# Kernel tuning notes

Hardware: AMD Instinct MI355X
Metric: run time of the kernel (lower is better)

The kernel has to match this reference:

```python
import jax, jax.numpy as jnp
import numpy as np

N_NODES = 100000
N_EDGES = 1600000
IN_DIM, HID_DIM, OUT_DIM = 128, 128, 47
BN_EPS = 1e-5


def setup_inputs() -> dict:
    key = jax.random.key(0)
    ks = jax.random.split(key, 12)
    x = jax.random.normal(ks[0], (N_NODES, IN_DIM), dtype=jnp.float32)
    edge_index = jax.random.randint(ks[1], (2, N_EDGES), 0, N_NODES, dtype=jnp.int32)
    def glorot(k, fan_in, fan_out):
        s = jnp.sqrt(6.0 / (fan_in + fan_out))
        return jax.random.uniform(k, (fan_in, fan_out), jnp.float32, -s, s)
    return {
        "x": x,
        "edge_index": edge_index,
        "W0": glorot(ks[2], IN_DIM, HID_DIM), "b0": jnp.zeros((HID_DIM,), jnp.float32),
        "W1": glorot(ks[3], HID_DIM, HID_DIM), "b1": jnp.zeros((HID_DIM,), jnp.float32),
        "W2": glorot(ks[4], HID_DIM, OUT_DIM), "b2": jnp.zeros((OUT_DIM,), jnp.float32),
        "g0": jnp.ones((HID_DIM,), jnp.float32), "be0": jnp.zeros((HID_DIM,), jnp.float32),
        "g1": jnp.ones((HID_DIM,), jnp.float32), "be1": jnp.zeros((HID_DIM,), jnp.float32),
    }


def _gcn_norm(edge_index, n_nodes):
    # add self-loops, compute sym-normalized edge weights (PyG GCNConv default)
    loop = jnp.arange(n_nodes, dtype=edge_index.dtype)
    src = jnp.concatenate([edge_index[0], loop])
    dst = jnp.concatenate([edge_index[1], loop])
    deg = jax.ops.segment_sum(jnp.ones_like(dst, dtype=jnp.float32), dst,
                              num_segments=n_nodes)
    dinv = jnp.where(deg > 0, jax.lax.rsqrt(deg), 0.0)
    norm = dinv[src] * dinv[dst]  # [E + N]
    return src, dst, norm


def _conv(x, W, b, src, dst, norm, n_nodes):
    h = x @ W                                   # [N, d_out]
    msg = h[src] * norm[:, None]                # gather + scale
    out = jax.ops.segment_sum(msg, dst, num_segments=n_nodes)
    return out + b


def _batchnorm(h, gamma, beta):
    mean = jnp.mean(h, axis=0)
    var = jnp.mean(jnp.square(h - mean), axis=0)  # biased var (torch BN)
    return (h - mean) * jax.lax.rsqrt(var + BN_EPS) * gamma + beta


def reference(x, edge_index, W0, b0, W1, b1, W2, b2, g0, be0, g1, be1):
    n = x.shape[0]
    src, dst, norm = _gcn_norm(edge_index, n)
    h = _conv(x, W0, b0, src, dst, norm, n)
    h = jax.nn.relu(_batchnorm(h, g0, be0))     # dropout = identity (eval)
    h = _conv(h, W1, b1, src, dst, norm, n)
    h = jax.nn.relu(_batchnorm(h, g1, be1))
    h = _conv(h, W2, b2, src, dst, norm, n)
    return jax.nn.log_softmax(h, axis=-1)
```

## Files before the change

### kernel.cpp

```cpp
#include <hip/hip_runtime.h>
#include <math.h>

#define N_NODES 100000
#define N_EDGES 1600000
#define HID 128
#define OUTD 47
#define OSTR 64

#define NPB 128
#define NB 782
#define BCAP 2560
#define CHUNK 2048
#define NCHB 782
#define CWB 64

typedef short bf16x8 __attribute__((ext_vector_type(8)));
typedef float f32x4 __attribute__((ext_vector_type(4)));

__device__ inline unsigned short f2bf(float x) {
    union { float f; unsigned int u; } v; v.f = x;
    unsigned int r = v.u + 0x7fffu + ((v.u >> 16) & 1u);
    return (unsigned short)(r >> 16);
}
__device__ inline float bf_lo(unsigned int u) { return __uint_as_float(u << 16); }
__device__ inline float bf_hi(unsigned int u) { return __uint_as_float(u & 0xffff0000u); }

__device__ inline unsigned int cvt_pk_bf16(float lo, float hi) {
    unsigned int r;
    asm("v_cvt_pk_bf16_f32 %0, %1, %2" : "=v"(r) : "v"(lo), "v"(hi));
    return r;
}

__device__ inline unsigned int src_chunk(unsigned int s) {
    return (s * 42950u) >> 28;
}


__global__ __launch_bounds__(256) void binA_k(
    const int* __restrict__ src, const int* __restrict__ dst,
    int* __restrict__ gcur, unsigned int* __restrict__ binned,
    const float* __restrict__ W0, const float* __restrict__ W1, const float* __restrict__ W2,
    unsigned short* __restrict__ Wt0, unsigned short* __restrict__ Wt1,
    unsigned short* __restrict__ Wt2)
{
    __shared__ unsigned int sortedL[CHUNK];
    __shared__ unsigned short bucketOf[CHUNK];
    __shared__ int cntL[NB];
    __shared__ int excL[NB];
    __shared__ int curL[NB];
    __shared__ int gposL[NB];
    __shared__ int partial[256];

    int t = threadIdx.x;

    if (blockIdx.x >= NCHB) {
        int i = (blockIdx.x - NCHB) * 256 + t;
        if (i < 16384) {
            int n = i >> 7, k = i & 127;
            Wt0[i] = f2bf(W0[k * 128 + n]);
            Wt1[i] = f2bf(W1[k * 128 + n]);
        }
        if (i < 64 * 128) {
            int n = i >> 7, k = i & 127;
            Wt2[i] = (n < OUTD) ? f2bf(W2[k * OUTD + n]) : (unsigned short)0;
        }
        return;
    }

    int e0 = blockIdx.x * CHUNK;

    for (int i = t; i < NB; i += 256) cntL[i] = 0;
    __syncthreads();

    for (int i = t; i < CHUNK; i += 256) {
        int e = e0 + i;
        if (e < N_EDGES) atomicAdd(&cntL[dst[e] >> 7], 1);
    }
    __syncthreads();

    int b4 = t * 4;
    int c0 = (b4 + 0 < NB) ? cntL[b4 + 0] : 0;
    int c1 = (b4 + 1 < NB) ? cntL[b4 + 1] : 0;
    int c2 = (b4 + 2 < NB) ? cntL[b4 + 2] : 0;
    int c3 = (b4 + 3 < NB) ? cntL[b4 + 3] : 0;
    int lsum = c0 + c1 + c2 + c3;
    partial[t] = lsum;
    __syncthreads();
    for (int off = 1; off < 256; off <<= 1) {
        int x = (t >= off) ? partial[t - off] : 0;
        __syncthreads();
        partial[t] += x;
        __syncthreads();
    }
    int pbase = partial[t] - lsum;
    if (b4 + 0 < NB) { excL[b4 + 0] = pbase;                curL[b4 + 0] = pbase; }
    if (b4 + 1 < NB) { excL[b4 + 1] = pbase + c0;           curL[b4 + 1] = pbase + c0; }
    if (b4 + 2 < NB) { excL[b4 + 2] = pbase + c0 + c1;      curL[b4 + 2] = pbase + c0 + c1; }
    if (b4 + 3 < NB) { excL[b4 + 3] = pbase + c0 + c1 + c2; curL[b4 + 3] = pbase + c0 + c1 + c2; }
    __syncthreads();

    int tot = partial[255];

    for (int i = t; i < CHUNK; i += 256) {
        int e = e0 + i;
        if (e < N_EDGES) {
            int d = dst[e];
            int s = src[e];
            int bkt = d >> 7;
            int pos = atomicAdd(&curL[bkt], 1);
            sortedL[pos] = ((unsigned int)s << 7) | (unsigned int)(d & 127);
            bucketOf[pos] = (unsigned short)bkt;
        }
    }
    __syncthreads();

    for (int b = t; b < NB; b += 256) {
        int c = cntL[b];
        gposL[b] = c ? atomicAdd(&gcur[b], c) : 0;
    }
    __syncthreads();

    for (int i = t; i < tot; i += 256) {
        unsigned int r = sortedL[i];
        int bkt = bucketOf[i];
        binned[(size_t)bkt * BCAP + gposL[bkt] + (i - excL[bkt])] = r;
    }
}


__global__ __launch_bounds__(256) void binB_k(
    const unsigned int* __restrict__ binned, const int* __restrict__ gcur,
    int2* __restrict__ rowse, float* __restrict__ dinv, int* __restrict__ colv)
{
    __shared__ unsigned int recL[BCAP];
    __shared__ int colL[BCAP];
    __shared__ int hist[2048];
    __shared__ int partial[256];

    int b = blockIdx.x, t = threadIdx.x;
    int cnt = gcur[b];
    int base = b * BCAP;
    const unsigned int* rp = binned + (size_t)b * BCAP;

    for (int i = t; i < 2048; i += 256) hist[i] = 0;
    __syncthreads();

    for (int i = t; i < cnt; i += 256) {
        unsigned int r = rp[i];
        recL[i] = r;
        unsigned int key = ((r & 127u) << 4) | src_chunk(r >> 7);
        atomicAdd(&hist[key], 1);
    }
    __syncthreads();

    int base8 = t * 8;
    int v[8], lsum = 0;
#pragma unroll
    for (int j = 0; j < 8; j++) { v[j] = hist[base8 + j]; lsum += v[j]; }
    partial[t] = lsum;
    __syncthreads();
    for (int off = 1; off < 256; off <<= 1) {
        int x = (t >= off) ? partial[t - off] : 0;
        __syncthreads();
        partial[t] += x;
        __syncthreads();
    }
    int run = partial[t] - lsum;
#pragma unroll
    for (int j = 0; j < 8; j++) { hist[base8 + j] = run; run += v[j]; }
    __syncthreads();

    if (t < NPB) {
        int node = b * NPB + t;
        if (node < N_NODES) {
            int start = hist[t << 4];
            int end = (t < NPB - 1) ? hist[(t + 1) << 4] : cnt;
            rowse[node] = make_int2(base + start, base + end);
            dinv[node] = rsqrtf((float)(end - start + 1));
        }
    }
    __syncthreads();

    for (int i = t; i < cnt; i += 256) {
        unsigned int r = recL[i];
        unsigned int key = ((r & 127u) << 4) | src_chunk(r >> 7);
        int pos = atomicAdd(&hist[key], 1);
        colL[pos] = (int)(r >> 7);
    }
    __syncthreads();
    for (int i = t; i < cnt; i += 256) colv[base + i] = colL[i];
}


template <int ABF16, int MODE, int NT, int OBF16>
__global__ __launch_bounds__(256) void gemm_k(
    const void* __restrict__ Ap, const unsigned short* __restrict__ Wt,
    const float* __restrict__ bnSum, const float* __restrict__ bnSq,
    const float* __restrict__ gam, const float* __restrict__ bet,
    const float* __restrict__ dinv, void* __restrict__ Outp,
    int ncols, int ostride)
{
    __shared__ unsigned short WtL[NT * 16][136];
    __shared__ float2 sST[128];

    int t = threadIdx.x;
    if (MODE) {
        if (t < 128) {
            float s_ = 0.f, q_ = 0.f;
            for (int sl = 0; sl < 64; sl++) {
                s_ += bnSum[sl * 128 + t];
                q_ += bnSq[sl * 128 + t];
            }
            float mean = s_ * (1.0f / N_NODES);
            float var = q_ * (1.0f / N_NODES) - mean * mean;
            float inv = rsqrtf(var + 1e-5f);
            float s = gam[t] * inv;
            sST[t] = make_float2(s, bet[t] - mean * s);
        }
    }

    const int TOT = NT * 16 * 128;
    for (int e = t * 8; e < TOT; e += 256 * 8) {
        int n = e >> 7, k = e & 127;
        uint4 v = *(const uint4*)(Wt + e);
        *(uint4*)&WtL[n][k] = v;
    }
    __syncthreads();

    int wave = t >> 6, lane = t & 63;
    int quad = lane >> 4, m16 = lane & 15;
    int rbase = blockIdx.x * 128 + wave * 32;

    uint4 av[2][4];
#pragma unroll
    for (int rt = 0; rt < 2; rt++) {
        int row = rbase + rt * 16 + m16;
        bool rv = (row < N_NODES);
        if (ABF16) {
            const uint4* ap = (const uint4*)((const unsigned short*)Ap + (size_t)row * 128);
#pragma unroll
            for (int kc = 0; kc < 4; kc++)
                av[rt][kc] = rv ? ap[kc * 4 + quad] : make_uint4(0, 0, 0, 0);
        } else {
            const float4* ap = (const float4*)((const float*)Ap + (size_t)row * 128);
            float4 f[8];
#pragma unroll
            for (int kc = 0; kc < 4; kc++) {
                f[2 * kc]     = rv ? ap[kc * 8 + quad * 2]     : make_float4(0.f, 0.f, 0.f, 0.f);
                f[2 * kc + 1] = rv ? ap[kc * 8 + quad * 2 + 1] : make_float4(0.f, 0.f, 0.f, 0.f);
            }
#pragma unroll
            for (int kc = 0; kc < 4; kc++) {
                uint4 v;
                v.x = cvt_pk_bf16(f[2 * kc].x, f[2 * kc].y);
                v.y = cvt_pk_bf16(f[2 * kc].z, f[2 * kc].w);
                v.z = cvt_pk_bf16(f[2 * kc + 1].x, f[2 * kc + 1].y);
                v.w = cvt_pk_bf16(f[2 * kc + 1].z, f[2 * kc + 1].w);
                av[rt][kc] = v;
            }
        }
    }

    f32x4 acc[2][NT];
#pragma unroll
    for (int rt = 0; rt < 2; rt++)
#pragma unroll
        for (int ct = 0; ct < NT; ct++) acc[rt][ct] = (f32x4){0.f, 0.f, 0.f, 0.f};

#pragma unroll
    for (int kc = 0; kc < 4; kc++) {
        int kb = kc * 32 + quad * 8;
        bf16x8 afrag[2];
#pragma unroll
        for (int rt = 0; rt < 2; rt++) {
            if (MODE) {
                unsigned int uu[4] = {av[rt][kc].x, av[rt][kc].y, av[rt][kc].z, av[rt][kc].w};
                unsigned int* up = (unsigned int*)&afrag[rt];
#pragma unroll
                for (int i = 0; i < 4; i++) {
                    int k0 = kb + 2 * i;
                    float2 sa = sST[k0], sb = sST[k0 + 1];
                    float lo = fmaxf(bf_lo(uu[i]) * sa.x + sa.y, 0.f);
                    float hi = fmaxf(bf_hi(uu[i]) * sb.x + sb.y, 0.f);
                    up[i] = cvt_pk_bf16(lo, hi);
                }
            } else {
                afrag[rt] = *(bf16x8*)&av[rt][kc];
            }
        }
#pragma unroll
        for (int ct = 0; ct < NT; ct++) {
            bf16x8 bfrag = *(bf16x8*)&WtL[ct * 16 + m16][kb];
#pragma unroll
            for (int rt = 0; rt < 2; rt++)
                acc[rt][ct] = __builtin_amdgcn_mfma_f32_16x16x32_bf16(
                    afrag[rt], bfrag, acc[rt][ct], 0, 0, 0);
        }
    }

#pragma unroll
    for (int rt = 0; rt < 2; rt++)
#pragma unroll
        for (int r = 0; r < 4; r++) {
            int row = rbase + rt * 16 + quad * 4 + r;
            if (row < N_NODES) {
                float d = dinv[row];
#pragma unroll
                for (int ct = 0; ct < NT; ct++) {
                    int c = ct * 16 + m16;
                    if (c < ncols) {
                        float val = acc[rt][ct][r] * d;
                        if (OBF16)
                            ((unsigned short*)Outp)[(size_t)row * ostride + c] =
                                (unsigned short)cvt_pk_bf16(val, 0.f);
                        else
                            ((float*)Outp)[(size_t)row * ostride + c] = val;
                    }
                }
            }
        }
}


__global__ __launch_bounds__(256) void agg_k(
    const unsigned int* __restrict__ H, const int2* __restrict__ rowse,
    const int* __restrict__ colv, const float* __restrict__ dinv,
    const float* __restrict__ bias,
    float* __restrict__ bnPS, float* __restrict__ bnPQ,
    unsigned int* __restrict__ out)
{
    __shared__ float red[2][4][16][9];

    int t = threadIdx.x;
    int gw = (blockIdx.x * 256 + t) >> 6;
    int lane = t & 63;
    int w = t >> 6;
    int q = lane >> 4;
    int c = lane & 15;
    int2 se = rowse[gw];
    int rp = se.x, re = se.y;
    const uint4* H4 = (const uint4*)H;

    float a0 = 0.f, a1 = 0.f, a2 = 0.f, a3 = 0.f;
    float a4 = 0.f, a5 = 0.f, a6 = 0.f, a7 = 0.f;
    if (q == 0) {
        uint4 u = H4[(size_t)gw * 16 + c];
        a0 = bf_lo(u.x); a1 = bf_hi(u.x); a2 = bf_lo(u.y); a3 = bf_hi(u.y);
        a4 = bf_lo(u.z); a5 = bf_hi(u.z); a6 = bf_lo(u.w); a7 = bf_hi(u.w);
    }

    for (int j0 = rp; j0 < re; j0 += 64) {
        int idx = (j0 + lane < re) ? colv[j0 + lane] : 0;
        int n = min(64, re - j0);
        int nq = n >> 2;
        int t4 = 0;
        for (; t4 + 1 < nq; t4 += 2) {
            int sa = __shfl(idx, 4 * t4 + q);
            int sb = __shfl(idx, 4 * t4 + 4 + q);
            uint4 ua = H4[(size_t)sa * 16 + c];
            uint4 ub = H4[(size_t)sb * 16 + c];
            a0 += bf_lo(ua.x) + bf_lo(ub.x);
            a1 += bf_hi(ua.x) + bf_hi(ub.x);
            a2 += bf_lo(ua.y) + bf_lo(ub.y);
            a3 += bf_hi(ua.y) + bf_hi(ub.y);
            a4 += bf_lo(ua.z) + bf_lo(ub.z);
            a5 += bf_hi(ua.z) + bf_hi(ub.z);
            a6 += bf_lo(ua.w) + bf_lo(ub.w);
            a7 += bf_hi(ua.w) + bf_hi(ub.w);
        }
        if (t4 < nq) {
            int sa = __shfl(idx, 4 * t4 + q);
            uint4 ua = H4[(size_t)sa * 16 + c];
            a0 += bf_lo(ua.x); a1 += bf_hi(ua.x);
            a2 += bf_lo(ua.y); a3 += bf_hi(ua.y);
            a4 += bf_lo(ua.z); a5 += bf_hi(ua.z);
            a6 += bf_lo(ua.w); a7 += bf_hi(ua.w);
        }
        int rem = n & 3;
        if (rem) {
            int sa = __shfl(idx, (n - rem) + q);
            if (q < rem) {
                uint4 ua = H4[(size_t)sa * 16 + c];
                a0 += bf_lo(ua.x); a1 += bf_hi(ua.x);
                a2 += bf_lo(ua.y); a3 += bf_hi(ua.y);
                a4 += bf_lo(ua.z); a5 += bf_hi(ua.z);
                a6 += bf_lo(ua.w); a7 += bf_hi(ua.w);
            }
        }
    }

    a0 += __shfl_xor(a0, 16); a0 += __shfl_xor(a0, 32);
    a1 += __shfl_xor(a1, 16); a1 += __shfl_xor(a1, 32);
    a2 += __shfl_xor(a2, 16); a2 += __shfl_xor(a2, 32);
    a3 += __shfl_xor(a3, 16); a3 += __shfl_xor(a3, 32);
    a4 += __shfl_xor(a4, 16); a4 += __shfl_xor(a4, 32);
    a5 += __shfl_xor(a5, 16); a5 += __shfl_xor(a5, 32);
    a6 += __shfl_xor(a6, 16); a6 += __shfl_xor(a6, 32);
    a7 += __shfl_xor(a7, 16); a7 += __shfl_xor(a7, 32);

    if (q == 0) {
        float d = dinv[gw];
        float4 ba = ((const float4*)bias)[2 * c];
        float4 bb = ((const float4*)bias)[2 * c + 1];
        float vv[8];
        vv[0] = a0 * d + ba.x; vv[1] = a1 * d + ba.y;
        vv[2] = a2 * d + ba.z; vv[3] = a3 * d + ba.w;
        vv[4] = a4 * d + bb.x; vv[5] = a5 * d + bb.y;
        vv[6] = a6 * d + bb.z; vv[7] = a7 * d + bb.w;
        uint4 r;
        r.x = cvt_pk_bf16(vv[0], vv[1]);
        r.y = cvt_pk_bf16(vv[2], vv[3]);
        r.z = cvt_pk_bf16(vv[4], vv[5]);
        r.w = cvt_pk_bf16(vv[6], vv[7]);
        ((uint4*)out)[(size_t)gw * 16 + c] = r;
#pragma unroll
        for (int k = 0; k < 8; k++) {
            red[0][w][c][k] = vv[k];
            red[1][w][c][k] = vv[k] * vv[k];
        }
    }
    __syncthreads();

    {
        int part = t >> 7;
        int ch = t & 127;
        int cc = ch >> 3, k = ch & 7;
        float s = red[part][0][cc][k] + red[part][1][cc][k]
                + red[part][2][cc][k] + red[part][3][cc][k];
        atomicAdd((part ? bnPQ : bnPS) + (blockIdx.x & 63) * 128 + ch, s);
    }
}


__global__ __launch_bounds__(256) void agg_out_k(
    const unsigned int* __restrict__ H, const int2* __restrict__ rowse,
    const int* __restrict__ colv, const float* __restrict__ dinv,
    const float* __restrict__ b2, float* __restrict__ out)
{
    int gw = (blockIdx.x * 256 + threadIdx.x) >> 6;
    int lane = threadIdx.x & 63;
    if (gw >= N_NODES) return;
    int q = lane >> 4;
    int c = lane & 15;
    bool ld = c < 12;
    int2 se = rowse[gw];
    int rp = se.x, re = se.y;
    const uint2* H2 = (const uint2*)H;

    float a0 = 0.f, a1 = 0.f, a2 = 0.f, a3 = 0.f;
    if (q == 0 && ld) {
        uint2 u = H2[(size_t)gw * 16 + c];
        a0 = bf_lo(u.x); a1 = bf_hi(u.x); a2 = bf_lo(u.y); a3 = bf_hi(u.y);
    }

    for (int j0 = rp; j0 < re; j0 += 64) {
        int idx = (j0 + lane < re) ? colv[j0 + lane] : 0;
        int n = min(64, re - j0);
        int nq = n >> 2;
        int t4 = 0;
        for (; t4 + 1 < nq; t4 += 2) {
            int sa = __shfl(idx, 4 * t4 + q);
            int sb = __shfl(idx, 4 * t4 + 4 + q);
            if (ld) {
                uint2 ua = H2[(size_t)sa * 16 + c];
                uint2 ub = H2[(size_t)sb * 16 + c];
                a0 += bf_lo(ua.x) + bf_lo(ub.x);
                a1 += bf_hi(ua.x) + bf_hi(ub.x);
                a2 += bf_lo(ua.y) + bf_lo(ub.y);
                a3 += bf_hi(ua.y) + bf_hi(ub.y);
            }
        }
        if (t4 < nq) {
            int sa = __shfl(idx, 4 * t4 + q);
            if (ld) {
                uint2 ua = H2[(size_t)sa * 16 + c];
                a0 += bf_lo(ua.x); a1 += bf_hi(ua.x);
                a2 += bf_lo(ua.y); a3 += bf_hi(ua.y);
            }
        }
        int rem = n & 3;
        if (rem) {
            int sa = __shfl(idx, (n - rem) + q);
            if (q < rem && ld) {
                uint2 ua = H2[(size_t)sa * 16 + c];
                a0 += bf_lo(ua.x); a1 += bf_hi(ua.x);
                a2 += bf_lo(ua.y); a3 += bf_hi(ua.y);
            }
        }
    }

    a0 += __shfl_xor(a0, 16); a0 += __shfl_xor(a0, 32);
    a1 += __shfl_xor(a1, 16); a1 += __shfl_xor(a1, 32);
    a2 += __shfl_xor(a2, 16); a2 += __shfl_xor(a2, 32);
    a3 += __shfl_xor(a3, 16); a3 += __shfl_xor(a3, 32);

    float d = dinv[gw];
    int ch = c * 4;
    float v0 = -INFINITY, v1 = -INFINITY, v2 = -INFINITY, v3 = -INFINITY;
    if (ld) {
        v0 = a0 * d + b2[ch];
        v1 = a1 * d + b2[ch + 1];
        v2 = a2 * d + b2[ch + 2];
        if (ch + 3 < OUTD) v3 = a3 * d + b2[ch + 3];
    }
    float m = fmaxf(fmaxf(v0, v1), fmaxf(v2, v3));
    m = fmaxf(m, __shfl_xor(m, 1));
    m = fmaxf(m, __shfl_xor(m, 2));
    m = fmaxf(m, __shfl_xor(m, 4));
    m = fmaxf(m, __shfl_xor(m, 8));
    float e = 0.f;
    if (ld) {
        e = __expf(v0 - m) + __expf(v1 - m) + __expf(v2 - m);
        if (ch + 3 < OUTD) e += __expf(v3 - m);
    }
    float sum = e;
    sum += __shfl_xor(sum, 1);
    sum += __shfl_xor(sum, 2);
    sum += __shfl_xor(sum, 4);
    sum += __shfl_xor(sum, 8);
    float ls = logf(sum);
    if (q == 0 && ld) {
        float* op = out + (size_t)gw * OUTD + ch;
        op[0] = v0 - m - ls;
        op[1] = v1 - m - ls;
        op[2] = v2 - m - ls;
        if (ch + 3 < OUTD) op[3] = v3 - m - ls;
    }
}


extern "C" void kernel_launch(void* const* d_in, const int* in_sizes, int n_in,
                              void* d_out, int out_size, void* d_ws, size_t ws_size,
                              hipStream_t stream)
{
    const float* x   = (const float*)d_in[0];
    const int*   ei  = (const int*)d_in[1];
    const float* W0  = (const float*)d_in[2];
    const float* b0  = (const float*)d_in[3];
    const float* W1  = (const float*)d_in[4];
    const float* b1  = (const float*)d_in[5];
    const float* W2  = (const float*)d_in[6];
    const float* b2  = (const float*)d_in[7];
    const float* g0  = (const float*)d_in[8];
    const float* be0 = (const float*)d_in[9];
    const float* g1  = (const float*)d_in[10];
    const float* be1 = (const float*)d_in[11];
    const int* srcv = ei;
    const int* dstv = ei + N_EDGES;

    char* w = (char*)d_ws;
    unsigned int* H0 = (unsigned int*)w;  w += (size_t)N_NODES * 128 * 2;
    unsigned int* H1 = (unsigned int*)w;  w += (size_t)N_NODES * 128 * 2;
    unsigned int* Hf = (unsigned int*)w;  w += (size_t)N_NODES * OSTR * 2;
    unsigned int* binned = (unsigned int*)w; w += (size_t)NB * BCAP * 4;
    int* colv = (int*)w;        w += (size_t)NB * BCAP * 4;
    unsigned short* Wt0 = (unsigned short*)w; w += 16384 * 2;
    unsigned short* Wt1 = (unsigned short*)w; w += 16384 * 2;
    unsigned short* Wt2 = (unsigned short*)w; w += 64 * 128 * 2;
    int2* rowse = (int2*)w;     w += (size_t)N_NODES * 8;
    float* dinv = (float*)w;    w += (size_t)N_NODES * 4;
    int* gcur = (int*)w;        w += 784 * 4;
    float* bnP0S = (float*)w;   w += 64 * 128 * 4;
    float* bnP0Q = (float*)w;   w += 64 * 128 * 4;
    float* bnP1S = (float*)w;   w += 64 * 128 * 4;
    float* bnP1Q = (float*)w;   w += 64 * 128 * 4;

    int gb = (N_NODES + 127) / 128;
    int ab = (N_NODES * 64 + 255) / 256;

    hipMemsetAsync(gcur, 0, 784 * 4 + 4 * 64 * 128 * 4, stream);

    binA_k<<<NCHB + CWB, 256, 0, stream>>>(srcv, dstv, gcur, binned,
                                           W0, W1, W2, Wt0, Wt1, Wt2);
    binB_k<<<NB, 256, 0, stream>>>(binned, gcur, rowse, dinv, colv);

    gemm_k<0, 0, 8, 1><<<gb, 256, 0, stream>>>(x, Wt0, nullptr, nullptr, nullptr, nullptr,
                                               dinv, H0, 128, 128);
    agg_k<<<ab, 256, 0, stream>>>(H0, rowse, colv, dinv, b0, bnP0S, bnP0Q, H1);

    gemm_k<1, 1, 8, 1><<<gb, 256, 0, stream>>>(H1, Wt1, bnP0S, bnP0Q, g0, be0,
                                               dinv, H0, 128, 128);
    agg_k<<<ab, 256, 0, stream>>>(H0, rowse, colv, dinv, b1, bnP1S, bnP1Q, H1);

    gemm_k<1, 1, 4, 1><<<gb, 256, 0, stream>>>(H1, Wt2, bnP1S, bnP1Q, g1, be1,
                                               dinv, Hf, 64, OSTR);
    agg_out_k<<<ab, 256, 0, stream>>>(Hf, rowse, colv, dinv, b2, (float*)d_out);
}
```

Measured before the change: 413.0 us.

## Drop LDS weight staging in GEMM and halve rows per block

The GEMM kernel no longer copies the transposed weight matrix into shared memory. Each MFMA now reads its B fragments straight from global memory, which should mostly hit in L2/L1. Each wave now handles 16 rows instead of 32, so blocks cover 64 rows and the grid doubles. The aim is to remove the per-block weight copy and barrier, cut LDS use, and raise occupancy. The cost is repeated global loads of the weights and half the reuse of each B fragment across row tiles.

Result: slower. 450.6 us (+9.1%).

```diff
diff --git a/kernel.cpp b/kernel.cpp
--- a/kernel.cpp
+++ b/kernel.cpp
@@ -200,7 +200,6 @@
     const float* __restrict__ dinv, void* __restrict__ Outp,
     int ncols, int ostride)
 {
-    __shared__ unsigned short WtL[NT * 16][136];
     __shared__ float2 sST[128];
 
     int t = threadIdx.x;
@@ -217,108 +216,88 @@
             float s = gam[t] * inv;
             sST[t] = make_float2(s, bet[t] - mean * s);
         }
-    }
-
-    const int TOT = NT * 16 * 128;
-    for (int e = t * 8; e < TOT; e += 256 * 8) {
-        int n = e >> 7, k = e & 127;
-        uint4 v = *(const uint4*)(Wt + e);
-        *(uint4*)&WtL[n][k] = v;
-    }
-    __syncthreads();
+        __syncthreads();
+    }
 
     int wave = t >> 6, lane = t & 63;
     int quad = lane >> 4, m16 = lane & 15;
-    int rbase = blockIdx.x * 128 + wave * 32;
-
-    uint4 av[2][4];
-#pragma unroll
-    for (int rt = 0; rt < 2; rt++) {
-        int row = rbase + rt * 16 + m16;
-        bool rv = (row < N_NODES);
-        if (ABF16) {
-            const uint4* ap = (const uint4*)((const unsigned short*)Ap + (size_t)row * 128);
-#pragma unroll
-            for (int kc = 0; kc < 4; kc++)
-                av[rt][kc] = rv ? ap[kc * 4 + quad] : make_uint4(0, 0, 0, 0);
-        } else {
-            const float4* ap = (const float4*)((const float*)Ap + (size_t)row * 128);
-            float4 f[8];
-#pragma unroll
-            for (int kc = 0; kc < 4; kc++) {
-                f[2 * kc]     = rv ? ap[kc * 8 + quad * 2]     : make_float4(0.f, 0.f, 0.f, 0.f);
-                f[2 * kc + 1] = rv ? ap[kc * 8 + quad * 2 + 1] : make_float4(0.f, 0.f, 0.f, 0.f);
-            }
-#pragma unroll
-            for (int kc = 0; kc < 4; kc++) {
-                uint4 v;
-                v.x = cvt_pk_bf16(f[2 * kc].x, f[2 * kc].y);
-                v.y = cvt_pk_bf16(f[2 * kc].z, f[2 * kc].w);
-                v.z = cvt_pk_bf16(f[2 * kc + 1].x, f[2 * kc + 1].y);
-                v.w = cvt_pk_bf16(f[2 * kc + 1].z, f[2 * kc + 1].w);
-                av[rt][kc] = v;
-            }
-        }
-    }
-
-    f32x4 acc[2][NT];
-#pragma unroll
-    for (int rt = 0; rt < 2; rt++)
-#pragma unroll
-        for (int ct = 0; ct < NT; ct++) acc[rt][ct] = (f32x4){0.f, 0.f, 0.f, 0.f};
+    int row0 = blockIdx.x * 64 + wave * 16;
+    int arow = row0 + m16;
+    bool rv = (arow < N_NODES);
+
+    uint4 av[4];
+    if (ABF16) {
+        const uint4* ap = (const uint4*)((const unsigned short*)Ap + (size_t)arow * 128);
+#pragma unroll
+        for (int kc = 0; kc < 4; kc++)
+            av[kc] = rv ? ap[kc * 4 + quad] : make_uint4(0, 0, 0, 0);
+    } else {
+        const float4* ap = (const float4*)((const float*)Ap + (size_t)arow * 128);
+        float4 f[8];
+#pragma unroll
+        for (int kc = 0; kc < 4; kc++) {
+            f[2 * kc]     = rv ? ap[kc * 8 + quad * 2]     : make_float4(0.f, 0.f, 0.f, 0.f);
+            f[2 * kc + 1] = rv ? ap[kc * 8 + quad * 2 + 1] : make_float4(0.f, 0.f, 0.f, 0.f);
+        }
+#pragma unroll
+        for (int kc = 0; kc < 4; kc++) {
+            uint4 v;
+            v.x = cvt_pk_bf16(f[2 * kc].x, f[2 * kc].y);
+            v.y = cvt_pk_bf16(f[2 * kc].z, f[2 * kc].w);
+            v.z = cvt_pk_bf16(f[2 * kc + 1].x, f[2 * kc + 1].y);
+            v.w = cvt_pk_bf16(f[2 * kc + 1].z, f[2 * kc + 1].w);
+            av[kc] = v;
+        }
+    }
+
+    f32x4 acc[NT];
+#pragma unroll
+    for (int ct = 0; ct < NT; ct++) acc[ct] = (f32x4){0.f, 0.f, 0.f, 0.f};
 
 #pragma unroll
     for (int kc = 0; kc < 4; kc++) {
         int kb = kc * 32 + quad * 8;
-        bf16x8 afrag[2];
-#pragma unroll
-        for (int rt = 0; rt < 2; rt++) {
-            if (MODE) {
-                unsigned int uu[4] = {av[rt][kc].x, av[rt][kc].y, av[rt][kc].z, av[rt][kc].w};
-                unsigned int* up = (unsigned int*)&afrag[rt];
-#pragma unroll
-                for (int i = 0; i < 4; i++) {
-                    int k0 = kb + 2 * i;
-                    float2 sa = sST[k0], sb = sST[k0 + 1];
-                    float lo = fmaxf(bf_lo(uu[i]) * sa.x + sa.y, 0.f);
-                    float hi = fmaxf(bf_hi(uu[i]) * sb.x + sb.y, 0.f);
-                    up[i] = cvt_pk_bf16(lo, hi);
+        bf16x8 afrag;
+        if (MODE) {
+            unsigned int uu[4] = {av[kc].x, av[kc].y, av[kc].z, av[kc].w};
+            unsigned int* up = (unsigned int*)&afrag;
+#pragma unroll
+            for (int i = 0; i < 4; i++) {
+                int k0 = kb + 2 * i;
+                float2 sa = sST[k0], sb = sST[k0 + 1];
+                float lo = fmaxf(bf_lo(uu[i]) * sa.x + sa.y, 0.f);
+                float hi = fmaxf(bf_hi(uu[i]) * sb.x + sb.y, 0.f);
+                up[i] = cvt_pk_bf16(lo, hi);
+            }
+        } else {
+            afrag = *(bf16x8*)&av[kc];
+        }
+#pragma unroll
+        for (int ct = 0; ct < NT; ct++) {
+            bf16x8 bfrag = *(const bf16x8*)(Wt + (size_t)(ct * 16 + m16) * 128 + kb);
+            acc[ct] = __builtin_amdgcn_mfma_f32_16x16x32_bf16(afrag, bfrag, acc[ct], 0, 0, 0);
+        }
+    }
+
+#pragma unroll
+    for (int r = 0; r < 4; r++) {
+        int orow = row0 + quad * 4 + r;
+        if (orow < N_NODES) {
+            float d = dinv[orow];
+#pragma unroll
+            for (int ct = 0; ct < NT; ct++) {
+                int c = ct * 16 + m16;
+                if (c < ncols) {
+                    float val = acc[ct][r] * d;
+                    if (OBF16)
+                        ((unsigned short*)Outp)[(size_t)orow * ostride + c] =
+                            (unsigned short)cvt_pk_bf16(val, 0.f);
+                    else
+                        ((float*)Outp)[(size_t)orow * ostride + c] = val;
                 }
-            } else {
-                afrag[rt] = *(bf16x8*)&av[rt][kc];
-            }
-        }
-#pragma unroll
-        for (int ct = 0; ct < NT; ct++) {
-            bf16x8 bfrag = *(bf16x8*)&WtL[ct * 16 + m16][kb];
-#pragma unroll
-            for (int rt = 0; rt < 2; rt++)
-                acc[rt][ct] = __builtin_amdgcn_mfma_f32_16x16x32_bf16(
-                    afrag[rt], bfrag, acc[rt][ct], 0, 0, 0);
-        }
-    }
-
-#pragma unroll
-    for (int rt = 0; rt < 2; rt++)
-#pragma unroll
-        for (int r = 0; r < 4; r++) {
-            int row = rbase + rt * 16 + quad * 4 + r;
-            if (row < N_NODES) {
-                float d = dinv[row];
-#pragma unroll
-                for (int ct = 0; ct < NT; ct++) {
-                    int c = ct * 16 + m16;
-                    if (c < ncols) {
-                        float val = acc[rt][ct][r] * d;
-                        if (OBF16)
-                            ((unsigned short*)Outp)[(size_t)row * ostride + c] =
-                                (unsigned short)cvt_pk_bf16(val, 0.f);
-                        else
-                            ((float*)Outp)[(size_t)row * ostride + c] = val;
-                    }
-                }
-            }
-        }
+            }
+        }
+    }
 }
 
 
@@ -565,7 +544,7 @@
     float* bnP1S = (float*)w;   w += 64 * 128 * 4;
     float* bnP1Q = (float*)w;   w += 64 * 128 * 4;
 
-    int gb = (N_NODES + 127) / 128;
+    int gb = (N_NODES + 63) / 64;
     int ab = (N_NODES * 64 + 255) / 256;
 
     hipMemsetAsync(gcur, 0, 784 * 4 + 4 * 64 * 128 * 4, stream);
```
